# Kernel optimization log

Hardware: AMD Instinct MI355X
Metric: run time of the kernel (lower is better)

The kernel has to match this reference:

```python
import jax, jax.numpy as jnp
import numpy as np

B, L, D, H = 8, 1024, 768, 12
HD = D // H
EPS = 1e-5
R_EPS = 1e-12  # numerical guard for r at coincident positions


def setup_inputs() -> dict:
    key = jax.random.key(0)
    ks = jax.random.split(key, 8)
    x = jax.random.normal(ks[0], (B, L, D), dtype=jnp.float32)
    # 32x32 patch grid coordinates, same for every batch element
    g = jnp.arange(32, dtype=jnp.float32)
    yy, xx = jnp.meshgrid(g, g, indexing='ij')
    pos = jnp.broadcast_to(jnp.stack([yy.ravel(), xx.ravel()], axis=-1), (B, L, 2))
    w_norm = jnp.ones((D,), dtype=jnp.float32)
    w_in = 0.02 * jax.random.normal(ks[1], (3 * D, D), dtype=jnp.float32)
    b_in = jnp.zeros((3 * D,), dtype=jnp.float32)
    w_out = 0.02 * jax.random.normal(ks[2], (D, D), dtype=jnp.float32)
    b_out = jnp.zeros((D,), dtype=jnp.float32)
    # bias params [H, 6] = (o, c, w, p, delta, m) per init_bias_params
    o = jnp.zeros((H,), dtype=jnp.float32)
    c = 1.0 + 0.3 * jax.random.uniform(ks[3], (H,), dtype=jnp.float32)
    w = jnp.ones((H,), dtype=jnp.float32)
    p = jnp.zeros((H,), dtype=jnp.float32)
    delta = jax.random.normal(ks[4], (H,), dtype=jnp.float32)
    m = jnp.ones((H,), dtype=jnp.float32)
    bias_params = jnp.stack([o, c, w, p, delta, m], axis=-1)
    return {"x": x, "pos": pos, "w_norm": w_norm, "w_in": w_in, "b_in": b_in,
            "w_out": w_out, "b_out": b_out, "bias_params": bias_params}


def _bias_grid(pos, bias_params):
    # pos: [B, L, 2] -> bias: [B, H, L, L]
    o, c, w, p, delta, m = [bias_params[:, i].reshape(1, H, 1, 1) for i in range(6)]
    dist = pos[:, :, None, :] - pos[:, None, :, :]          # [B, Lq, Lk, 2]
    theta = jnp.arctan2(dist[..., 1], dist[..., 0])[:, None]  # [B, 1, Lq, Lk]
    r = jnp.sqrt(jnp.sum(dist * dist, axis=-1) + R_EPS)[:, None]
    term1 = jax.nn.relu(r - o) ** jnp.abs(c)
    term2 = 1.0 - jnp.abs(jnp.tanh(delta)) * (jnp.cos((theta - p) * w * 0.5) ** 2) ** jnp.abs(m)
    return term1 * term2


def reference(x, pos, w_norm, w_in, b_in, w_out, b_out, bias_params):
    bias = _bias_grid(pos, bias_params)                      # [B, H, L, L]
    # RMSNorm
    xn = x * jax.lax.rsqrt(jnp.mean(x * x, axis=-1, keepdims=True) + EPS) * w_norm
    qkv = xn @ w_in.T + b_in                                 # [B, L, 3D]
    q, k, v = jnp.split(qkv, 3, axis=-1)
    def heads(t):
        return t.reshape(B, L, H, HD).transpose(0, 2, 1, 3)  # [B, H, L, HD]
    q, k, v = heads(q), heads(k), heads(v)
    scores = jnp.einsum('bhqd,bhkd->bhqk', q, k) / jnp.sqrt(jnp.float32(HD)) + bias
    attn = jax.nn.softmax(scores, axis=-1)
    o = jnp.einsum('bhqk,bhkd->bhqd', attn, v)
    o = o.transpose(0, 2, 1, 3).reshape(B, L, D)
    return o @ w_out.T + b_out
```

## Files before the change

### kernel.cpp

```cpp
#include <hip/hip_runtime.h>

#define BB 8
#define LL 1024
#define DD 768
#define HH 12
#define HD 64

typedef short s16x8 __attribute__((ext_vector_type(8)));
typedef float f32x4 __attribute__((ext_vector_type(4)));
typedef unsigned int u32x4 __attribute__((ext_vector_type(4)));

static __device__ __forceinline__ unsigned short f2bf(float f){
  unsigned int u = __builtin_bit_cast(unsigned int, f);
  u = (u + 0x7FFFu + ((u >> 16) & 1u)) >> 16;
  return (unsigned short)u;
}

static __device__ __forceinline__ unsigned int cvtpk_bf(float a, float b){
  unsigned int r;
  asm("v_cvt_pk_bf16_f32 %0, %1, %2" : "=v"(r) : "v"(a), "v"(b));
  return r;
}

static __device__ __forceinline__ void swap32(unsigned int& a, unsigned int& b){
  asm("v_permlane32_swap_b32 %0, %1" : "+v"(a), "+v"(b));
}
static __device__ __forceinline__ void swap16(unsigned int& a, unsigned int& b){
  asm("v_permlane16_swap_b32 %0, %1" : "+v"(a), "+v"(b));
}

static __device__ __forceinline__ float hexp2(float x){
#if __has_builtin(__builtin_amdgcn_exp2f)
  return __builtin_amdgcn_exp2f(x);
#else
  return exp2f(x);
#endif
}

static __device__ __forceinline__ f32x4 mfma16(s16x8 a, s16x8 b, f32x4 c){
  return __builtin_amdgcn_mfma_f32_16x16x32_bf16(a, b, c, 0, 0, 0);
}

static __device__ __forceinline__ void gld_lds16(const void* g, void* l){
  __builtin_amdgcn_global_load_lds(
      (const __attribute__((address_space(1))) void*)g,
      (__attribute__((address_space(3))) void*)l, 16, 0, 0);
}

__global__ __launch_bounds__(256) void prep_kernel(const float* __restrict__ w_in,
                                                   unsigned short* __restrict__ winb,
                                                   const float* __restrict__ w_out,
                                                   unsigned short* __restrict__ woutb,
                                                   const float* __restrict__ bp,
                                                   float* __restrict__ table){
  int bid = blockIdx.x, tid = threadIdx.x;
  if (bid < 1728){
    int i = bid*256 + tid;
    float4 v = ((const float4*)w_in)[i];
    ushort4 o;
    o.x = f2bf(v.x); o.y = f2bf(v.y); o.z = f2bf(v.z); o.w = f2bf(v.w);
    ((ushort4*)winb)[i] = o;
  } else if (bid < 2304){
    int i = (bid - 1728)*256 + tid;
    float4 v = ((const float4*)w_out)[i];
    ushort4 o;
    o.x = f2bf(v.x); o.y = f2bf(v.y); o.z = f2bf(v.z); o.w = f2bf(v.w);
    ((ushort4*)woutb)[i] = o;
  } else {
    int idx = (bid - 2304)*256 + tid;
    if (idx >= HH*3969) return;
    int hh = idx/3969, rem = idx - hh*3969;
    int dy = rem/63 - 31, dx = rem%63 - 31;
    float o  = bp[hh*6+0], c = bp[hh*6+1], w = bp[hh*6+2];
    float p  = bp[hh*6+3], dl = bp[hh*6+4], m = bp[hh*6+5];
    float theta = atan2f((float)dx, (float)dy);
    float r = sqrtf((float)(dy*dy + dx*dx) + 1e-12f);
    float t1 = powf(fmaxf(r - o, 0.0f), fabsf(c));
    float co = cosf((theta - p)*w*0.5f);
    float t2 = 1.0f - fabsf(tanhf(dl))*powf(co*co, fabsf(m));
    table[idx] = t1*t2*1.44269504f;
  }
}

__global__ __launch_bounds__(64) void bmax_kernel(const float* __restrict__ table,
                                                  float* __restrict__ bmax){
  int qy = blockIdx.x, h = blockIdx.y;
  __shared__ float m1[63];
  int t = threadIdx.x;
  const float* tb = table + h*3969;
  if (t < 63){
    float m = -3.0e38f;
    #pragma unroll 4
    for (int row = qy; row < qy + 32; row++) m = fmaxf(m, tb[row*63 + t]);
    m1[t] = m;
  }
  __syncthreads();
  if (t < 32){
    float m = -3.0e38f;
    #pragma unroll 4
    for (int c = t; c < t + 32; c++) m = fmaxf(m, m1[c]);
    bmax[(h*32 + qy)*32 + t] = m;
  }
}

__global__ __launch_bounds__(256) void rmsnorm_kernel(const float* __restrict__ x,
                                                      const float* __restrict__ wn,
                                                      unsigned short* __restrict__ xn){
  int row = blockIdx.x, t = threadIdx.x;
  const float* xr = x + (size_t)row*DD;
  float v0 = xr[t], v1 = xr[t+256], v2 = xr[t+512];
  float ss = v0*v0 + v1*v1 + v2*v2;
  #pragma unroll
  for (int m = 1; m < 64; m <<= 1) ss += __shfl_xor(ss, m, 64);
  __shared__ float red[4];
  if ((t & 63) == 0) red[t >> 6] = ss;
  __syncthreads();
  float tot = red[0] + red[1] + red[2] + red[3];
  float sc = rsqrtf(tot*(1.0f/DD) + 1e-5f);
  unsigned short* xo = xn + (size_t)row*DD;
  xo[t]     = f2bf(v0*sc*wn[t]);
  xo[t+256] = f2bf(v1*sc*wn[t+256]);
  xo[t+512] = f2bf(v2*sc*wn[t+512]);
}

static __device__ __forceinline__ void storeC(float* p, float v){ *p = v; }
static __device__ __forceinline__ void storeC(unsigned short* p, float v){ *p = f2bf(v); }

template<int MODE, int TN, typename OutT>
__global__ __launch_bounds__(256) void gemm_bt_kernel(const unsigned short* __restrict__ A,
                                                      const unsigned short* __restrict__ B,
                                                      const float* __restrict__ bias,
                                                      OutT* __restrict__ C,
                                                      unsigned short* __restrict__ qp,
                                                      unsigned short* __restrict__ kp,
                                                      unsigned short* __restrict__ vp,
                                                      int M, int N, int K){
  constexpr int NT = TN/32;
  constexpr int SMEM_BYTES = 192*(128 + TN);
  __shared__ __align__(16) char smem[SMEM_BYTES];
  unsigned short* As = (unsigned short*)smem;
  unsigned short* Bs = (unsigned short*)(smem + 3*128*32*2);
  int tid = threadIdx.x;
  int w = tid >> 6, lane = tid & 63, quad = lane >> 4, col = lane & 15;
  int wm = (w >> 1)*64, wn = (w & 1)*(TN/2);
  int bm = blockIdx.x*128, bn = blockIdx.y*TN;

  int srow = lane >> 2;
  int schunk = (((lane & 3) ^ ((lane >> 3) & 3)))*8;
  const unsigned short* ga0 = A + (size_t)(bm + w*32 + srow)*K + schunk;
  const unsigned short* ga1 = ga0 + (size_t)16*K;
  const unsigned short* gb0 = B + (size_t)(bn + w*(TN/4) + srow)*K + schunk;
  const unsigned short* gb1 = gb0 + (size_t)16*K;

  auto stage = [&](int t, int bi){
    int kk = t*32;
    gld_lds16(ga0 + kk, As + bi*4096 + (w*32)*32);
    gld_lds16(ga1 + kk, As + bi*4096 + (w*32 + 16)*32);
    gld_lds16(gb0 + kk, Bs + bi*(TN*32) + (w*(TN/4))*32);
    if (TN == 128) gld_lds16(gb1 + kk, Bs + bi*(TN*32) + (w*32 + 16)*32);
  };

  f32x4 acc[4][NT];
  #pragma unroll
  for (int mt = 0; mt < 4; mt++)
    #pragma unroll
    for (int nt = 0; nt < NT; nt++) acc[mt][nt] = (f32x4){0.f,0.f,0.f,0.f};

  stage(0, 0);
  stage(1, 1);

  int rsw = (col >> 1) & 3;
  int rchunk = (quad ^ rsw)*8;

  int KT = K >> 5;
  int buf = 0, nbuf = 2;
  for (int t = 0; t < KT; t++){
    if (t < KT - 1){
      if (TN == 128) asm volatile("s_waitcnt vmcnt(4)" ::: "memory");
      else           asm volatile("s_waitcnt vmcnt(3)" ::: "memory");
    } else {
      asm volatile("s_waitcnt vmcnt(0)" ::: "memory");
    }
    __builtin_amdgcn_s_barrier();
    asm volatile("" ::: "memory");
    if (t + 2 < KT) stage(t + 2, nbuf);
    s16x8 af[4], bfr[NT];
    #pragma unroll
    for (int mt = 0; mt < 4; mt++)
      af[mt] = *(const s16x8*)&As[buf*4096 + (wm + mt*16 + col)*32 + rchunk];
    #pragma unroll
    for (int nt = 0; nt < NT; nt++)
      bfr[nt] = *(const s16x8*)&Bs[buf*(TN*32) + (wn + nt*16 + col)*32 + rchunk];
    #pragma unroll
    for (int mt = 0; mt < 4; mt++)
      #pragma unroll
      for (int nt = 0; nt < NT; nt++)
        acc[mt][nt] = mfma16(af[mt], bfr[nt], acc[mt][nt]);
    buf  = (buf  == 2) ? 0 : buf  + 1;
    nbuf = (nbuf == 2) ? 0 : nbuf + 1;
  }

  if (MODE == 1){
    __syncthreads();
    unsigned short* Ct = (unsigned short*)smem;
    #pragma unroll
    for (int mt = 0; mt < 4; mt++)
      #pragma unroll
      for (int nt = 0; nt < NT; nt++){
        int cc = wn + nt*16 + col;
        float bv = bias[bn + cc];
        #pragma unroll
        for (int r = 0; r < 4; r++){
          int row = wm + mt*16 + quad*4 + r;
          Ct[row*136 + cc] = f2bf(acc[mt][nt][r] + bv);
        }
      }
    __syncthreads();
    #pragma unroll
    for (int e = 0; e < 8; e++){
      int id = e*256 + tid;
      int row = id >> 4, ch = id & 15;
      s16x8 val = *(const s16x8*)&Ct[row*136 + ch*8];
      int rw = bm + row;
      int cl0 = bn + ch*8;
      int part = cl0 >= 1536 ? 2 : (cl0 >= 768 ? 1 : 0);
      int hd = cl0 - part*768;
      int hh2 = hd >> 6, d0 = hd & 63;
      int bb = rw >> 10, l = rw & 1023;
      size_t base = (((size_t)bb*HH + hh2)*LL + l)*64;
      if (part == 0)      *(s16x8*)(qp + base + d0) = val;
      else if (part == 1) *(s16x8*)(kp + base + (((d0>>3) ^ (l&7)) << 3)) = val;
      else                *(s16x8*)(vp + base + d0) = val;
    }
  } else {
    __syncthreads();
    float* Cf = (float*)smem;
    #pragma unroll
    for (int mt = 0; mt < 4; mt++)
      #pragma unroll
      for (int nt = 0; nt < NT; nt++){
        int cc = wn + nt*16 + col;
        float bv = bias[bn + cc];
        #pragma unroll
        for (int r = 0; r < 4; r++){
          int row = wm + mt*16 + quad*4 + r;
          Cf[row*68 + cc] = acc[mt][nt][r] + bv;
        }
      }
    __syncthreads();
    #pragma unroll
    for (int e = 0; e < 8; e++){
      int id = e*256 + tid;
      int row = id >> 4, ch = id & 15;
      float4 val = *(const float4*)&Cf[row*68 + ch*4];
      *(float4*)&C[(size_t)(bm + row)*N + bn + ch*4] = val;
    }
  }
}

__global__ __launch_bounds__(256) void vtrans_kernel(const unsigned short* __restrict__ vp,
                                                     unsigned short* __restrict__ vt2){
  int jt = blockIdx.x, bh = blockIdx.y;
  __shared__ unsigned short tile[32][68];
  int t = threadIdx.x;
  const unsigned short* src = vp + ((size_t)bh*LL + jt*32)*64;
  #pragma unroll
  for (int e = 0; e < 8; e++){
    int lin = t + 256*e;
    tile[lin >> 6][lin & 63] = src[lin];
  }
  __syncthreads();
  unsigned short* dst = vt2 + ((size_t)bh*32 + jt)*2048;
  #pragma unroll
  for (int e = 0; e < 8; e++){
    int lin = t + 256*e;
    dst[lin] = tile[lin & 31][lin >> 5];
  }
}

__global__ __launch_bounds__(128) void attn_kernel(const unsigned short* __restrict__ qp,
                                                   const unsigned short* __restrict__ kp,
                                                   const unsigned short* __restrict__ vt2,
                                                   const float* __restrict__ table,
                                                   const float* __restrict__ bmax,
                                                   const float* __restrict__ pos,
                                                   unsigned short* __restrict__ o_out){
  int i = blockIdx.x;
  int bh = (i >> 7)*8 + (i & 7);
  int qt = (i >> 3) & 7;
  int wp = (i >> 6) & 1;
  int b = bh/HH, h = bh - b*HH;
  int tid = threadIdx.x, w = tid >> 6, lane = tid & 63, quad = lane >> 4, col = lane & 15;
  __shared__ float tl[3969];

  const unsigned short* kgp = kp  + (size_t)bh*65536;
  const unsigned short* vgp = vt2 + (size_t)bh*65536;

  int sw = col & 7;
  int k_r0 = col*64 + ((quad ^ sw) << 3);
  int k_r1 = col*64 + (((quad + 4) ^ sw) << 3);
  int v_r  = col*32 + quad*8;

  s16x8 kA[4], vA[4], kB[4], vB[4];
  auto issue = [&](int t, s16x8 (&k)[4], s16x8 (&v)[4]){
    const unsigned short* kt = kgp + t*2048;
    const unsigned short* vt = vgp + t*2048;
    k[0] = *(const s16x8*)(kt + k_r0);
    k[1] = *(const s16x8*)(kt + k_r1);
    k[2] = *(const s16x8*)(kt + 1024 + k_r0);
    k[3] = *(const s16x8*)(kt + 1024 + k_r1);
    v[0] = *(const s16x8*)(vt + v_r);
    v[1] = *(const s16x8*)(vt + v_r + 512);
    v[2] = *(const s16x8*)(vt + v_r + 1024);
    v[3] = *(const s16x8*)(vt + v_r + 1536);
  };
  issue(0, kA, vA);
  issue(1, kB, vB);

  for (int j = tid; j < 3969; j += 128) tl[j] = table[h*3969 + j];
  const float* pb = pos + (size_t)b*2048;

  int qw = qt*128 + (wp*2 + w)*32;
  const unsigned short* qpb = qp + (size_t)bh*65536;
  s16x8 qa[2][2];
  int cq[2];
  f32x4 zb[2];
  #pragma unroll
  for (int g = 0; g < 2; g++){
    int q = qw + g*16 + col;
    size_t qo = (size_t)q*64 + quad*8;
    qa[g][0] = *(const s16x8*)(qpb + qo);
    qa[g][1] = *(const s16x8*)(qpb + qo + 32);
    int qy = __float2int_rn(pb[q*2]);
    int qx = __float2int_rn(pb[q*2 + 1]);
    cq[g] = qy*63 + qx + 1984 - quad*4;
    float neg = -5.5451774445f * bmax[(h*32 + qy)*32 + qx];
    zb[g] = (f32x4){neg, neg, neg, neg};
  }

  s16x8 ones;
  #pragma unroll
  for (int e = 0; e < 8; e++) ones[e] = (short)0x3F80;

  f32x4 o[2][4];
  f32x4 l_acc[2];
  #pragma unroll
  for (int g = 0; g < 2; g++){
    #pragma unroll
    for (int nt = 0; nt < 4; nt++) o[g][nt] = (f32x4){0.f,0.f,0.f,0.f};
    l_acc[g] = (f32x4){0.f,0.f,0.f,0.f};
  }

  __syncthreads();

  auto step = [&](int t, s16x8 (&k)[4], s16x8 (&v)[4]){
    int kyt = 63*t;
    #pragma unroll
    for (int g = 0; g < 2; g++){
      __builtin_amdgcn_s_setprio(1);
      f32x4 s_lo = mfma16(k[0], qa[g][0], zb[g]);  s_lo = mfma16(k[1], qa[g][1], s_lo);
      f32x4 s_hi = mfma16(k[2], qa[g][0], zb[g]);  s_hi = mfma16(k[3], qa[g][1], s_hi);
      __builtin_amdgcn_s_setprio(0);
      int base = cq[g] - kyt;
      float pl[4], ph[4];
      #pragma unroll
      for (int r = 0; r < 4; r++){
        pl[r] = hexp2(__builtin_fmaf(s_lo[r], 0.18033688f, tl[base - r]));
        ph[r] = hexp2(__builtin_fmaf(s_hi[r], 0.18033688f, tl[base - r - 16]));
      }
      unsigned int wA = cvtpk_bf(pl[0], pl[1]);
      unsigned int wB = cvtpk_bf(pl[2], pl[3]);
      unsigned int wC = cvtpk_bf(ph[0], ph[1]);
      unsigned int wD = cvtpk_bf(ph[2], ph[3]);
      swap32(wA, wC);  swap32(wB, wD);
      swap16(wA, wC);  swap16(wB, wD);
      u32x4 pv4; pv4.x = wA; pv4.y = wB; pv4.z = wC; pv4.w = wD;
      s16x8 pf = __builtin_bit_cast(s16x8, pv4);
      __builtin_amdgcn_s_setprio(1);
      l_acc[g] = mfma16(ones, pf, l_acc[g]);
      o[g][0] = mfma16(v[0], pf, o[g][0]);
      o[g][1] = mfma16(v[1], pf, o[g][1]);
      o[g][2] = mfma16(v[2], pf, o[g][2]);
      o[g][3] = mfma16(v[3], pf, o[g][3]);
      __builtin_amdgcn_s_setprio(0);
    }
  };

  for (int t = 0; t < 32; t += 2){
    step(t, kA, vA);
    if (t + 2 < 32) issue(t + 2, kA, vA);
    step(t + 1, kB, vB);
    if (t + 3 < 32) issue(t + 3, kB, vB);
  }

  #pragma unroll
  for (int g = 0; g < 2; g++){
    float inv = 1.0f / l_acc[g][0];
    int q = qw + g*16 + col;
    unsigned short* orow = o_out + (size_t)(b*LL + q)*DD + h*64;
    #pragma unroll
    for (int nt = 0; nt < 4; nt++){
      uint2 pkd;
      pkd.x = cvtpk_bf(o[g][nt][0]*inv, o[g][nt][1]*inv);
      pkd.y = cvtpk_bf(o[g][nt][2]*inv, o[g][nt][3]*inv);
      *(uint2*)&orow[nt*16 + quad*4] = pkd;
    }
  }
}

extern "C" void kernel_launch(void* const* d_in, const int* in_sizes, int n_in,
                              void* d_out, int out_size, void* d_ws, size_t ws_size,
                              hipStream_t stream){
  const float* x      = (const float*)d_in[0];
  const float* pos    = (const float*)d_in[1];
  const float* w_norm = (const float*)d_in[2];
  const float* w_in   = (const float*)d_in[3];
  const float* b_in   = (const float*)d_in[4];
  const float* w_out  = (const float*)d_in[5];
  const float* b_out  = (const float*)d_in[6];
  const float* bp     = (const float*)d_in[7];

  char* ws = (char*)d_ws;
  unsigned short* xn    = (unsigned short*)(ws);
  unsigned short* winb  = (unsigned short*)(ws + 12582912);
  unsigned short* woutb = (unsigned short*)(ws + 16121856);
  unsigned short* qpb   = (unsigned short*)(ws + 17301504);
  unsigned short* kpb   = (unsigned short*)(ws + 29884416);
  unsigned short* vpb   = (unsigned short*)(ws + 42467328);
  unsigned short* vt2b  = (unsigned short*)(ws + 55050240);
  float*          table = (float*)        (ws + 67633152);
  unsigned short* ob    = (unsigned short*)(ws + 67823664);
  float*          bmaxp = (float*)        (ws);

  prep_kernel<<<dim3(2491), dim3(256), 0, stream>>>(w_in, winb, w_out, woutb, bp, table);
  rmsnorm_kernel<<<dim3(BB*LL), dim3(256), 0, stream>>>(x, w_norm, xn);
  gemm_bt_kernel<1, 128, unsigned short><<<dim3(64, 18), dim3(256), 0, stream>>>(
      xn, winb, b_in, (unsigned short*)nullptr, qpb, kpb, vpb, BB*LL, 3*DD, DD);
  bmax_kernel<<<dim3(32, HH), dim3(64), 0, stream>>>(table, bmaxp);
  vtrans_kernel<<<dim3(32, BB*HH), dim3(256), 0, stream>>>(vpb, vt2b);
  attn_kernel<<<dim3(1536), dim3(128), 0, stream>>>(qpb, kpb, vt2b, table, bmaxp, pos, ob);
  gemm_bt_kernel<0, 64, float><<<dim3(64, 12), dim3(256), 0, stream>>>(
      ob, woutb, b_out, (float*)d_out, nullptr, nullptr, nullptr, BB*LL, DD, DD);
}
```

Measured before the change: 224.7 us.

## Split attention keys across waves, merge partials, and fuse small prep kernels

The attention kernel now gives each block one 32-query tile and splits the 32 key tiles between its two waves. Each wave handles 16 key tiles, and the partial outputs and row sums are combined through LDS before the final normalisation. This doubles the attention grid to get more parallelism and shorter per-wave loops, at the cost of an extra LDS exchange and two barriers. The setprio hints are dropped. Separately, rmsnorm is fused into the prep launch and bmax is fused with the V transpose, cutting the launch count from seven to five.

```diff
diff --git a/kernel.cpp b/kernel.cpp
--- a/kernel.cpp
+++ b/kernel.cpp
@@ -47,27 +47,46 @@
       (__attribute__((address_space(3))) void*)l, 16, 0, 0);
 }
 
-__global__ __launch_bounds__(256) void prep_kernel(const float* __restrict__ w_in,
-                                                   unsigned short* __restrict__ winb,
-                                                   const float* __restrict__ w_out,
-                                                   unsigned short* __restrict__ woutb,
-                                                   const float* __restrict__ bp,
-                                                   float* __restrict__ table){
-  int bid = blockIdx.x, tid = threadIdx.x;
-  if (bid < 1728){
-    int i = bid*256 + tid;
+__global__ __launch_bounds__(256) void prep_norm_kernel(const float* __restrict__ x,
+                                                        const float* __restrict__ wn,
+                                                        unsigned short* __restrict__ xn,
+                                                        const float* __restrict__ w_in,
+                                                        unsigned short* __restrict__ winb,
+                                                        const float* __restrict__ w_out,
+                                                        unsigned short* __restrict__ woutb,
+                                                        const float* __restrict__ bp,
+                                                        float* __restrict__ table){
+  __shared__ float red[4];
+  int bid = blockIdx.x, t = threadIdx.x;
+  if (bid < 8192){
+    int row = bid;
+    const float* xr = x + (size_t)row*DD;
+    float v0 = xr[t], v1 = xr[t+256], v2 = xr[t+512];
+    float ss = v0*v0 + v1*v1 + v2*v2;
+    #pragma unroll
+    for (int m = 1; m < 64; m <<= 1) ss += __shfl_xor(ss, m, 64);
+    if ((t & 63) == 0) red[t >> 6] = ss;
+    __syncthreads();
+    float tot = red[0] + red[1] + red[2] + red[3];
+    float sc = rsqrtf(tot*(1.0f/DD) + 1e-5f);
+    unsigned short* xo = xn + (size_t)row*DD;
+    xo[t]     = f2bf(v0*sc*wn[t]);
+    xo[t+256] = f2bf(v1*sc*wn[t+256]);
+    xo[t+512] = f2bf(v2*sc*wn[t+512]);
+  } else if (bid < 8192 + 1728){
+    int i = (bid - 8192)*256 + t;
     float4 v = ((const float4*)w_in)[i];
     ushort4 o;
     o.x = f2bf(v.x); o.y = f2bf(v.y); o.z = f2bf(v.z); o.w = f2bf(v.w);
     ((ushort4*)winb)[i] = o;
-  } else if (bid < 2304){
-    int i = (bid - 1728)*256 + tid;
+  } else if (bid < 8192 + 2304){
+    int i = (bid - 8192 - 1728)*256 + t;
     float4 v = ((const float4*)w_out)[i];
     ushort4 o;
     o.x = f2bf(v.x); o.y = f2bf(v.y); o.z = f2bf(v.z); o.w = f2bf(v.w);
     ((ushort4*)woutb)[i] = o;
   } else {
-    int idx = (bid - 2304)*256 + tid;
+    int idx = (bid - 8192 - 2304)*256 + t;
     if (idx >= HH*3969) return;
     int hh = idx/3969, rem = idx - hh*3969;
     int dy = rem/63 - 31, dx = rem%63 - 31;
@@ -82,49 +101,48 @@
   }
 }
 
-__global__ __launch_bounds__(64) void bmax_kernel(const float* __restrict__ table,
-                                                  float* __restrict__ bmax){
-  int qy = blockIdx.x, h = blockIdx.y;
-  __shared__ float m1[63];
-  int t = threadIdx.x;
-  const float* tb = table + h*3969;
-  if (t < 63){
-    float m = -3.0e38f;
-    #pragma unroll 4
-    for (int row = qy; row < qy + 32; row++) m = fmaxf(m, tb[row*63 + t]);
-    m1[t] = m;
-  }
-  __syncthreads();
-  if (t < 32){
-    float m = -3.0e38f;
-    #pragma unroll 4
-    for (int c = t; c < t + 32; c++) m = fmaxf(m, m1[c]);
-    bmax[(h*32 + qy)*32 + t] = m;
-  }
-}
-
-__global__ __launch_bounds__(256) void rmsnorm_kernel(const float* __restrict__ x,
-                                                      const float* __restrict__ wn,
-                                                      unsigned short* __restrict__ xn){
-  int row = blockIdx.x, t = threadIdx.x;
-  const float* xr = x + (size_t)row*DD;
-  float v0 = xr[t], v1 = xr[t+256], v2 = xr[t+512];
-  float ss = v0*v0 + v1*v1 + v2*v2;
-  #pragma unroll
-  for (int m = 1; m < 64; m <<= 1) ss += __shfl_xor(ss, m, 64);
-  __shared__ float red[4];
-  if ((t & 63) == 0) red[t >> 6] = ss;
-  __syncthreads();
-  float tot = red[0] + red[1] + red[2] + red[3];
-  float sc = rsqrtf(tot*(1.0f/DD) + 1e-5f);
-  unsigned short* xo = xn + (size_t)row*DD;
-  xo[t]     = f2bf(v0*sc*wn[t]);
-  xo[t+256] = f2bf(v1*sc*wn[t+256]);
-  xo[t+512] = f2bf(v2*sc*wn[t+512]);
-}
-
-static __device__ __forceinline__ void storeC(float* p, float v){ *p = v; }
-static __device__ __forceinline__ void storeC(unsigned short* p, float v){ *p = f2bf(v); }
+__global__ __launch_bounds__(256) void post_kernel(const float* __restrict__ table,
+                                                   float* __restrict__ bmax,
+                                                   const unsigned short* __restrict__ vp,
+                                                   unsigned short* __restrict__ vt2){
+  __shared__ __align__(16) char psmem[32*68*2];
+  int bid = blockIdx.x, t = threadIdx.x;
+  if (bid < 3072){
+    unsigned short (*tile)[68] = (unsigned short(*)[68])psmem;
+    int jt = bid & 31, bh = bid >> 5;
+    const unsigned short* src = vp + ((size_t)bh*LL + jt*32)*64;
+    #pragma unroll
+    for (int e = 0; e < 8; e++){
+      int lin = t + 256*e;
+      tile[lin >> 6][lin & 63] = src[lin];
+    }
+    __syncthreads();
+    unsigned short* dst = vt2 + ((size_t)bh*32 + jt)*2048;
+    #pragma unroll
+    for (int e = 0; e < 8; e++){
+      int lin = t + 256*e;
+      dst[lin] = tile[lin & 31][lin >> 5];
+    }
+  } else {
+    float* m1 = (float*)psmem;
+    int idx = bid - 3072;
+    int qy = idx & 31, h = idx >> 5;
+    const float* tb = table + h*3969;
+    if (t < 63){
+      float m = -3.0e38f;
+      #pragma unroll 4
+      for (int row = qy; row < qy + 32; row++) m = fmaxf(m, tb[row*63 + t]);
+      m1[t] = m;
+    }
+    __syncthreads();
+    if (t < 32){
+      float m = -3.0e38f;
+      #pragma unroll 4
+      for (int c = t; c < t + 32; c++) m = fmaxf(m, m1[c]);
+      bmax[(h*32 + qy)*32 + t] = m;
+    }
+  }
+}
 
 template<int MODE, int TN, typename OutT>
 __global__ __launch_bounds__(256) void gemm_bt_kernel(const unsigned short* __restrict__ A,
@@ -258,26 +276,6 @@
   }
 }
 
-__global__ __launch_bounds__(256) void vtrans_kernel(const unsigned short* __restrict__ vp,
-                                                     unsigned short* __restrict__ vt2){
-  int jt = blockIdx.x, bh = blockIdx.y;
-  __shared__ unsigned short tile[32][68];
-  int t = threadIdx.x;
-  const unsigned short* src = vp + ((size_t)bh*LL + jt*32)*64;
-  #pragma unroll
-  for (int e = 0; e < 8; e++){
-    int lin = t + 256*e;
-    tile[lin >> 6][lin & 63] = src[lin];
-  }
-  __syncthreads();
-  unsigned short* dst = vt2 + ((size_t)bh*32 + jt)*2048;
-  #pragma unroll
-  for (int e = 0; e < 8; e++){
-    int lin = t + 256*e;
-    dst[lin] = tile[lin & 31][lin >> 5];
-  }
-}
-
 __global__ __launch_bounds__(128) void attn_kernel(const unsigned short* __restrict__ qp,
                                                    const unsigned short* __restrict__ kp,
                                                    const unsigned short* __restrict__ vt2,
@@ -286,9 +284,8 @@
                                                    const float* __restrict__ pos,
                                                    unsigned short* __restrict__ o_out){
   int i = blockIdx.x;
-  int bh = (i >> 7)*8 + (i & 7);
-  int qt = (i >> 3) & 7;
-  int wp = (i >> 6) & 1;
+  int bh = (i >> 8)*8 + (i & 7);
+  int qtile = (i >> 3) & 31;
   int b = bh/HH, h = bh - b*HH;
   int tid = threadIdx.x, w = tid >> 6, lane = tid & 63, quad = lane >> 4, col = lane & 15;
   __shared__ float tl[3969];
@@ -300,6 +297,8 @@
   int k_r0 = col*64 + ((quad ^ sw) << 3);
   int k_r1 = col*64 + (((quad + 4) ^ sw) << 3);
   int v_r  = col*32 + quad*8;
+
+  int t0 = w*16;
 
   s16x8 kA[4], vA[4], kB[4], vB[4];
   auto issue = [&](int t, s16x8 (&k)[4], s16x8 (&v)[4]){
@@ -314,13 +313,13 @@
     v[2] = *(const s16x8*)(vt + v_r + 1024);
     v[3] = *(const s16x8*)(vt + v_r + 1536);
   };
-  issue(0, kA, vA);
-  issue(1, kB, vB);
+  issue(t0, kA, vA);
+  issue(t0 + 1, kB, vB);
 
   for (int j = tid; j < 3969; j += 128) tl[j] = table[h*3969 + j];
   const float* pb = pos + (size_t)b*2048;
 
-  int qw = qt*128 + (wp*2 + w)*32;
+  int qw = qtile*32;
   const unsigned short* qpb = qp + (size_t)bh*65536;
   s16x8 qa[2][2];
   int cq[2];
@@ -357,10 +356,8 @@
     int kyt = 63*t;
     #pragma unroll
     for (int g = 0; g < 2; g++){
-      __builtin_amdgcn_s_setprio(1);
       f32x4 s_lo = mfma16(k[0], qa[g][0], zb[g]);  s_lo = mfma16(k[1], qa[g][1], s_lo);
       f32x4 s_hi = mfma16(k[2], qa[g][0], zb[g]);  s_hi = mfma16(k[3], qa[g][1], s_hi);
-      __builtin_amdgcn_s_setprio(0);
       int base = cq[g] - kyt;
       float pl[4], ph[4];
       #pragma unroll
@@ -376,34 +373,52 @@
       swap16(wA, wC);  swap16(wB, wD);
       u32x4 pv4; pv4.x = wA; pv4.y = wB; pv4.z = wC; pv4.w = wD;
       s16x8 pf = __builtin_bit_cast(s16x8, pv4);
-      __builtin_amdgcn_s_setprio(1);
       l_acc[g] = mfma16(ones, pf, l_acc[g]);
       o[g][0] = mfma16(v[0], pf, o[g][0]);
       o[g][1] = mfma16(v[1], pf, o[g][1]);
       o[g][2] = mfma16(v[2], pf, o[g][2]);
       o[g][3] = mfma16(v[3], pf, o[g][3]);
-      __builtin_amdgcn_s_setprio(0);
     }
   };
 
-  for (int t = 0; t < 32; t += 2){
+  for (int tt = 0; tt < 16; tt += 2){
+    int t = t0 + tt;
     step(t, kA, vA);
-    if (t + 2 < 32) issue(t + 2, kA, vA);
+    if (tt + 2 < 16) issue(t + 2, kA, vA);
     step(t + 1, kB, vB);
-    if (t + 3 < 32) issue(t + 3, kB, vB);
-  }
-
-  #pragma unroll
-  for (int g = 0; g < 2; g++){
-    float inv = 1.0f / l_acc[g][0];
-    int q = qw + g*16 + col;
-    unsigned short* orow = o_out + (size_t)(b*LL + q)*DD + h*64;
-    #pragma unroll
-    for (int nt = 0; nt < 4; nt++){
-      uint2 pkd;
-      pkd.x = cvtpk_bf(o[g][nt][0]*inv, o[g][nt][1]*inv);
-      pkd.y = cvtpk_bf(o[g][nt][2]*inv, o[g][nt][3]*inv);
-      *(uint2*)&orow[nt*16 + quad*4] = pkd;
+    if (tt + 3 < 16) issue(t + 3, kB, vB);
+  }
+
+  __syncthreads();
+  float* cb = (float*)tl;
+  if (w == 1){
+    float* p = cb + lane*37;
+    #pragma unroll
+    for (int g = 0; g < 2; g++){
+      #pragma unroll
+      for (int nt = 0; nt < 4; nt++)
+        #pragma unroll
+        for (int r = 0; r < 4; r++) p[g*17 + nt*4 + r] = o[g][nt][r];
+      p[g*17 + 16] = l_acc[g][0];
+    }
+  }
+  __syncthreads();
+  if (w == 0){
+    const float* p = cb + lane*37;
+    #pragma unroll
+    for (int g = 0; g < 2; g++){
+      float inv = 1.0f / (l_acc[g][0] + p[g*17 + 16]);
+      int q = qw + g*16 + col;
+      unsigned short* orow = o_out + (size_t)(b*LL + q)*DD + h*64;
+      #pragma unroll
+      for (int nt = 0; nt < 4; nt++){
+        uint2 pkd;
+        pkd.x = cvtpk_bf((o[g][nt][0] + p[g*17 + nt*4 + 0])*inv,
+                         (o[g][nt][1] + p[g*17 + nt*4 + 1])*inv);
+        pkd.y = cvtpk_bf((o[g][nt][2] + p[g*17 + nt*4 + 2])*inv,
+                         (o[g][nt][3] + p[g*17 + nt*4 + 3])*inv);
+        *(uint2*)&orow[nt*16 + quad*4] = pkd;
+      }
     }
   }
 }
@@ -432,13 +447,12 @@
   unsigned short* ob    = (unsigned short*)(ws + 67823664);
   float*          bmaxp = (float*)        (ws);
 
-  prep_kernel<<<dim3(2491), dim3(256), 0, stream>>>(w_in, winb, w_out, woutb, bp, table);
-  rmsnorm_kernel<<<dim3(BB*LL), dim3(256), 0, stream>>>(x, w_norm, xn);
+  prep_norm_kernel<<<dim3(8192 + 2491), dim3(256), 0, stream>>>(
+      x, w_norm, xn, w_in, winb, w_out, woutb, bp, table);
   gemm_bt_kernel<1, 128, unsigned short><<<dim3(64, 18), dim3(256), 0, stream>>>(
       xn, winb, b_in, (unsigned short*)nullptr, qpb, kpb, vpb, BB*LL, 3*DD, DD);
-  bmax_kernel<<<dim3(32, HH), dim3(64), 0, stream>>>(table, bmaxp);
-  vtrans_kernel<<<dim3(32, BB*HH), dim3(256), 0, stream>>>(vpb, vt2b);
-  attn_kernel<<<dim3(1536), dim3(128), 0, stream>>>(qpb, kpb, vt2b, table, bmaxp, pos, ob);
+  post_kernel<<<dim3(3072 + 384), dim3(256), 0, stream>>>(table, bmaxp, vpb, vt2b);
+  attn_kernel<<<dim3(3072), dim3(128), 0, stream>>>(qpb, kpb, vt2b, table, bmaxp, pos, ob);
   gemm_bt_kernel<0, 64, float><<<dim3(64, 12), dim3(256), 0, stream>>>(
       ob, woutb, b_out, (float*)d_out, nullptr, nullptr, nullptr, BB*LL, DD, DD);
 }
```

Measured after the change: 225.6 us. No clear change (+0.4%).

## Fuse V transpose into QKV GEMM epilogue and merge prep with RMSNorm

Applied to the files above, without the earlier changes.

The QKV GEMM epilogue now writes V directly in the transposed tiled layout the attention kernel reads, which removes the separate vtrans kernel and its round trip of V through global memory. RMSNorm and the weight/table prep are merged into one launch to save a kernel launch. The s_setprio hints around the MFMAs in the attention loop are also removed, which may change how waves interleave. The new V epilogue stores through a transposed LDS layout, which can cause more bank conflicts.

```diff
diff --git a/kernel.cpp b/kernel.cpp
--- a/kernel.cpp
+++ b/kernel.cpp
@@ -47,27 +47,46 @@
       (__attribute__((address_space(3))) void*)l, 16, 0, 0);
 }
 
-__global__ __launch_bounds__(256) void prep_kernel(const float* __restrict__ w_in,
-                                                   unsigned short* __restrict__ winb,
-                                                   const float* __restrict__ w_out,
-                                                   unsigned short* __restrict__ woutb,
-                                                   const float* __restrict__ bp,
-                                                   float* __restrict__ table){
-  int bid = blockIdx.x, tid = threadIdx.x;
-  if (bid < 1728){
-    int i = bid*256 + tid;
+__global__ __launch_bounds__(256) void prep_norm_kernel(const float* __restrict__ x,
+                                                        const float* __restrict__ wn,
+                                                        unsigned short* __restrict__ xn,
+                                                        const float* __restrict__ w_in,
+                                                        unsigned short* __restrict__ winb,
+                                                        const float* __restrict__ w_out,
+                                                        unsigned short* __restrict__ woutb,
+                                                        const float* __restrict__ bp,
+                                                        float* __restrict__ table){
+  __shared__ float red[4];
+  int bid = blockIdx.x, t = threadIdx.x;
+  if (bid < 8192){
+    int row = bid;
+    const float* xr = x + (size_t)row*DD;
+    float v0 = xr[t], v1 = xr[t+256], v2 = xr[t+512];
+    float ss = v0*v0 + v1*v1 + v2*v2;
+    #pragma unroll
+    for (int m = 1; m < 64; m <<= 1) ss += __shfl_xor(ss, m, 64);
+    if ((t & 63) == 0) red[t >> 6] = ss;
+    __syncthreads();
+    float tot = red[0] + red[1] + red[2] + red[3];
+    float sc = rsqrtf(tot*(1.0f/DD) + 1e-5f);
+    unsigned short* xo = xn + (size_t)row*DD;
+    xo[t]     = f2bf(v0*sc*wn[t]);
+    xo[t+256] = f2bf(v1*sc*wn[t+256]);
+    xo[t+512] = f2bf(v2*sc*wn[t+512]);
+  } else if (bid < 8192 + 1728){
+    int i = (bid - 8192)*256 + t;
     float4 v = ((const float4*)w_in)[i];
     ushort4 o;
     o.x = f2bf(v.x); o.y = f2bf(v.y); o.z = f2bf(v.z); o.w = f2bf(v.w);
     ((ushort4*)winb)[i] = o;
-  } else if (bid < 2304){
-    int i = (bid - 1728)*256 + tid;
+  } else if (bid < 8192 + 2304){
+    int i = (bid - 8192 - 1728)*256 + t;
     float4 v = ((const float4*)w_out)[i];
     ushort4 o;
     o.x = f2bf(v.x); o.y = f2bf(v.y); o.z = f2bf(v.z); o.w = f2bf(v.w);
     ((ushort4*)woutb)[i] = o;
   } else {
-    int idx = (bid - 2304)*256 + tid;
+    int idx = (bid - 8192 - 2304)*256 + t;
     if (idx >= HH*3969) return;
     int hh = idx/3969, rem = idx - hh*3969;
     int dy = rem/63 - 31, dx = rem%63 - 31;
@@ -103,29 +122,6 @@
   }
 }
 
-__global__ __launch_bounds__(256) void rmsnorm_kernel(const float* __restrict__ x,
-                                                      const float* __restrict__ wn,
-                                                      unsigned short* __restrict__ xn){
-  int row = blockIdx.x, t = threadIdx.x;
-  const float* xr = x + (size_t)row*DD;
-  float v0 = xr[t], v1 = xr[t+256], v2 = xr[t+512];
-  float ss = v0*v0 + v1*v1 + v2*v2;
-  #pragma unroll
-  for (int m = 1; m < 64; m <<= 1) ss += __shfl_xor(ss, m, 64);
-  __shared__ float red[4];
-  if ((t & 63) == 0) red[t >> 6] = ss;
-  __syncthreads();
-  float tot = red[0] + red[1] + red[2] + red[3];
-  float sc = rsqrtf(tot*(1.0f/DD) + 1e-5f);
-  unsigned short* xo = xn + (size_t)row*DD;
-  xo[t]     = f2bf(v0*sc*wn[t]);
-  xo[t+256] = f2bf(v1*sc*wn[t+256]);
-  xo[t+512] = f2bf(v2*sc*wn[t+512]);
-}
-
-static __device__ __forceinline__ void storeC(float* p, float v){ *p = v; }
-static __device__ __forceinline__ void storeC(unsigned short* p, float v){ *p = f2bf(v); }
-
 template<int MODE, int TN, typename OutT>
 __global__ __launch_bounds__(256) void gemm_bt_kernel(const unsigned short* __restrict__ A,
                                                       const unsigned short* __restrict__ B,
@@ -133,7 +129,7 @@
                                                       OutT* __restrict__ C,
                                                       unsigned short* __restrict__ qp,
                                                       unsigned short* __restrict__ kp,
-                                                      unsigned short* __restrict__ vp,
+                                                      unsigned short* __restrict__ vt2,
                                                       int M, int N, int K){
   constexpr int NT = TN/32;
   constexpr int SMEM_BYTES = 192*(128 + TN);
@@ -203,34 +199,61 @@
   if (MODE == 1){
     __syncthreads();
     unsigned short* Ct = (unsigned short*)smem;
-    #pragma unroll
-    for (int mt = 0; mt < 4; mt++)
-      #pragma unroll
-      for (int nt = 0; nt < NT; nt++){
-        int cc = wn + nt*16 + col;
-        float bv = bias[bn + cc];
+    if (bn >= 1536){
+      #pragma unroll
+      for (int mt = 0; mt < 4; mt++)
         #pragma unroll
-        for (int r = 0; r < 4; r++){
-          int row = wm + mt*16 + quad*4 + r;
-          Ct[row*136 + cc] = f2bf(acc[mt][nt][r] + bv);
+        for (int nt = 0; nt < NT; nt++){
+          int cc = wn + nt*16 + col;
+          float bv = bias[bn + cc];
+          #pragma unroll
+          for (int r = 0; r < 4; r++){
+            int row = wm + mt*16 + quad*4 + r;
+            Ct[cc*136 + row] = f2bf(acc[mt][nt][r] + bv);
+          }
         }
+      __syncthreads();
+      int bb = bm >> 10;
+      #pragma unroll
+      for (int e = 0; e < 8; e++){
+        int id = e*256 + tid;
+        int dcol = id >> 4, rowch = id & 15;
+        s16x8 val = *(const s16x8*)&Ct[dcol*136 + rowch*8];
+        int cl = bn + dcol - 1536;
+        int h = cl >> 6, d = cl & 63;
+        int l = bm + rowch*8;
+        size_t base = ((size_t)(bb*HH + h))*65536 + (size_t)((l >> 5) & 31)*2048;
+        *(s16x8*)(vt2 + base + d*32 + (l & 31)) = val;
       }
-    __syncthreads();
-    #pragma unroll
-    for (int e = 0; e < 8; e++){
-      int id = e*256 + tid;
-      int row = id >> 4, ch = id & 15;
-      s16x8 val = *(const s16x8*)&Ct[row*136 + ch*8];
-      int rw = bm + row;
-      int cl0 = bn + ch*8;
-      int part = cl0 >= 1536 ? 2 : (cl0 >= 768 ? 1 : 0);
-      int hd = cl0 - part*768;
-      int hh2 = hd >> 6, d0 = hd & 63;
-      int bb = rw >> 10, l = rw & 1023;
-      size_t base = (((size_t)bb*HH + hh2)*LL + l)*64;
-      if (part == 0)      *(s16x8*)(qp + base + d0) = val;
-      else if (part == 1) *(s16x8*)(kp + base + (((d0>>3) ^ (l&7)) << 3)) = val;
-      else                *(s16x8*)(vp + base + d0) = val;
+    } else {
+      #pragma unroll
+      for (int mt = 0; mt < 4; mt++)
+        #pragma unroll
+        for (int nt = 0; nt < NT; nt++){
+          int cc = wn + nt*16 + col;
+          float bv = bias[bn + cc];
+          #pragma unroll
+          for (int r = 0; r < 4; r++){
+            int row = wm + mt*16 + quad*4 + r;
+            Ct[row*136 + cc] = f2bf(acc[mt][nt][r] + bv);
+          }
+        }
+      __syncthreads();
+      #pragma unroll
+      for (int e = 0; e < 8; e++){
+        int id = e*256 + tid;
+        int row = id >> 4, ch = id & 15;
+        s16x8 val = *(const s16x8*)&Ct[row*136 + ch*8];
+        int rw = bm + row;
+        int cl0 = bn + ch*8;
+        int part = cl0 >= 768 ? 1 : 0;
+        int hd = cl0 - part*768;
+        int hh2 = hd >> 6, d0 = hd & 63;
+        int bb = rw >> 10, l = rw & 1023;
+        size_t base = (((size_t)bb*HH + hh2)*LL + l)*64;
+        if (part == 0) *(s16x8*)(qp + base + d0) = val;
+        else           *(s16x8*)(kp + base + (((d0>>3) ^ (l&7)) << 3)) = val;
+      }
     }
   } else {
     __syncthreads();
@@ -255,26 +278,6 @@
       float4 val = *(const float4*)&Cf[row*68 + ch*4];
       *(float4*)&C[(size_t)(bm + row)*N + bn + ch*4] = val;
     }
-  }
-}
-
-__global__ __launch_bounds__(256) void vtrans_kernel(const unsigned short* __restrict__ vp,
-                                                     unsigned short* __restrict__ vt2){
-  int jt = blockIdx.x, bh = blockIdx.y;
-  __shared__ unsigned short tile[32][68];
-  int t = threadIdx.x;
-  const unsigned short* src = vp + ((size_t)bh*LL + jt*32)*64;
-  #pragma unroll
-  for (int e = 0; e < 8; e++){
-    int lin = t + 256*e;
-    tile[lin >> 6][lin & 63] = src[lin];
-  }
-  __syncthreads();
-  unsigned short* dst = vt2 + ((size_t)bh*32 + jt)*2048;
-  #pragma unroll
-  for (int e = 0; e < 8; e++){
-    int lin = t + 256*e;
-    dst[lin] = tile[lin & 31][lin >> 5];
   }
 }
 
@@ -357,10 +360,8 @@
     int kyt = 63*t;
     #pragma unroll
     for (int g = 0; g < 2; g++){
-      __builtin_amdgcn_s_setprio(1);
       f32x4 s_lo = mfma16(k[0], qa[g][0], zb[g]);  s_lo = mfma16(k[1], qa[g][1], s_lo);
       f32x4 s_hi = mfma16(k[2], qa[g][0], zb[g]);  s_hi = mfma16(k[3], qa[g][1], s_hi);
-      __builtin_amdgcn_s_setprio(0);
       int base = cq[g] - kyt;
       float pl[4], ph[4];
       #pragma unroll
@@ -376,13 +377,11 @@
       swap16(wA, wC);  swap16(wB, wD);
       u32x4 pv4; pv4.x = wA; pv4.y = wB; pv4.z = wC; pv4.w = wD;
       s16x8 pf = __builtin_bit_cast(s16x8, pv4);
-      __builtin_amdgcn_s_setprio(1);
       l_acc[g] = mfma16(ones, pf, l_acc[g]);
       o[g][0] = mfma16(v[0], pf, o[g][0]);
       o[g][1] = mfma16(v[1], pf, o[g][1]);
       o[g][2] = mfma16(v[2], pf, o[g][2]);
       o[g][3] = mfma16(v[3], pf, o[g][3]);
-      __builtin_amdgcn_s_setprio(0);
     }
   };
 
@@ -426,18 +425,16 @@
   unsigned short* woutb = (unsigned short*)(ws + 16121856);
   unsigned short* qpb   = (unsigned short*)(ws + 17301504);
   unsigned short* kpb   = (unsigned short*)(ws + 29884416);
-  unsigned short* vpb   = (unsigned short*)(ws + 42467328);
   unsigned short* vt2b  = (unsigned short*)(ws + 55050240);
   float*          table = (float*)        (ws + 67633152);
   unsigned short* ob    = (unsigned short*)(ws + 67823664);
   float*          bmaxp = (float*)        (ws);
 
-  prep_kernel<<<dim3(2491), dim3(256), 0, stream>>>(w_in, winb, w_out, woutb, bp, table);
-  rmsnorm_kernel<<<dim3(BB*LL), dim3(256), 0, stream>>>(x, w_norm, xn);
+  prep_norm_kernel<<<dim3(8192 + 2491), dim3(256), 0, stream>>>(
+      x, w_norm, xn, w_in, winb, w_out, woutb, bp, table);
   gemm_bt_kernel<1, 128, unsigned short><<<dim3(64, 18), dim3(256), 0, stream>>>(
-      xn, winb, b_in, (unsigned short*)nullptr, qpb, kpb, vpb, BB*LL, 3*DD, DD);
+      xn, winb, b_in, (unsigned short*)nullptr, qpb, kpb, vt2b, BB*LL, 3*DD, DD);
   bmax_kernel<<<dim3(32, HH), dim3(64), 0, stream>>>(table, bmaxp);
-  vtrans_kernel<<<dim3(32, BB*HH), dim3(256), 0, stream>>>(vpb, vt2b);
   attn_kernel<<<dim3(1536), dim3(128), 0, stream>>>(qpb, kpb, vt2b, table, bmaxp, pos, ob);
   gemm_bt_kernel<0, 64, float><<<dim3(64, 12), dim3(256), 0, stream>>>(
       ob, woutb, b_out, (float*)d_out, nullptr, nullptr, nullptr, BB*LL, DD, DD);
```

New measurement: 218.3 us. -2.9%, faster.
